# Kernel tuning notes

Hardware: AMD Instinct MI355X
Metric: run time of the kernel (lower is better)

Reference implementation:

```python
import jax, jax.numpy as jnp
import numpy as np


def _gcn_conv(x, W, b, src, dst, num_nodes):
    # PyG GCNConv: linear transform, add self-loops, symmetric normalization,
    # scatter-sum aggregation, then bias.
    h = x @ W  # [N, out]
    loop = jnp.arange(num_nodes, dtype=src.dtype)
    s = jnp.concatenate([src, loop])
    d = jnp.concatenate([dst, loop])
    deg = jax.ops.segment_sum(jnp.ones_like(s, dtype=h.dtype), d, num_segments=num_nodes)
    dinv = jnp.where(deg > 0, jax.lax.rsqrt(deg), 0.0)
    norm = dinv[s] * dinv[d]  # [E+N]
    msgs = h[s] * norm[:, None]  # gather + scale
    out = jax.ops.segment_sum(msgs, d, num_segments=num_nodes)
    return out + b


def setup_inputs() -> dict:
    key = jax.random.key(0)
    k1, k2, k3, k4 = jax.random.split(key, 4)
    N, F_in, H, C, E = 100000, 512, 16, 40, 3200000
    node_feature = jax.random.normal(k1, (N, F_in), dtype=jnp.float32)
    W1 = jax.random.normal(k2, (F_in, H), dtype=jnp.float32) * (1.0 / np.sqrt(F_in))
    b1 = jnp.zeros((H,), dtype=jnp.float32)
    W2 = jax.random.normal(k3, (H, C), dtype=jnp.float32) * (1.0 / np.sqrt(H))
    b2 = jnp.zeros((C,), dtype=jnp.float32)
    edge_index = jax.random.randint(k4, (2, E), 0, N, dtype=jnp.int64)
    return {"node_feature": node_feature, "W1": W1, "b1": b1,
            "W2": W2, "b2": b2, "edge_index": edge_index}


def reference(node_feature, W1, b1, W2, b2, edge_index):
    # Inference path: F.dropout(training=False) is identity.
    N = node_feature.shape[0]
    src, dst = edge_index[0], edge_index[1]
    x = jax.nn.elu(_gcn_conv(node_feature, W1, b1, src, dst, N))
    x = _gcn_conv(x, W2, b2, src, dst, N)
    return jax.nn.log_softmax(x, axis=1)
```

## Files before the change

### kernel.cpp

```cpp
#include <hip/hip_runtime.h>
#include <hip/hip_bf16.h>
#include <math.h>

typedef __attribute__((ext_vector_type(8))) short bf16x8;
typedef __attribute__((ext_vector_type(4))) float f32x4;

#define CAP 8192

__device__ __forceinline__ unsigned pk_bf16(float lo, float hi) {
    unsigned a = __float_as_uint(lo), b = __float_as_uint(hi);
    unsigned alo = (a + 0x7fffu + ((a >> 16) & 1u)) >> 16;
    unsigned bhi = (b + 0x7fffu + ((b >> 16) & 1u)) >> 16;
    return alo | (bhi << 16);
}
__device__ __forceinline__ float bf_lo(unsigned u) { return __uint_as_float(u << 16); }
__device__ __forceinline__ float bf_hi(unsigned u) { return __uint_as_float(u & 0xffff0000u); }


__global__ __launch_bounds__(256) void k_place1(
    const int* __restrict__ src, const int* __restrict__ dst,
    int* __restrict__ gcur, unsigned* __restrict__ ebuf,
    int E, int B, int CHUNK)
{
    __shared__ int hist[1024];
    __shared__ int curb[1024];
    int tid = threadIdx.x, b = blockIdx.x;
    for (int j = tid; j < B; j += 256) hist[j] = 0;
    __syncthreads();
    int e0 = b * CHUNK, e1 = min(e0 + CHUNK, E);
    for (int i = e0 + tid * 4; i < e1; i += 1024) {
        if (i + 3 < e1) {
            int4 d4 = *(const int4*)(dst + i);
            atomicAdd(&hist[d4.x >> 7], 1);
            atomicAdd(&hist[d4.y >> 7], 1);
            atomicAdd(&hist[d4.z >> 7], 1);
            atomicAdd(&hist[d4.w >> 7], 1);
        } else {
            for (int k = i; k < e1; ++k) atomicAdd(&hist[dst[k] >> 7], 1);
        }
    }
    __syncthreads();
    for (int j = tid; j < B; j += 256) {
        int h = hist[j];
        curb[j] = h ? atomicAdd(&gcur[j], h) : 0;
    }
    __syncthreads();
    for (int i = e0 + tid * 4; i < e1; i += 1024) {
        if (i + 3 < e1) {
            int4 d4 = *(const int4*)(dst + i);
            int4 s4 = *(const int4*)(src + i);
            int p0 = atomicAdd(&curb[d4.x >> 7], 1);
            int p1 = atomicAdd(&curb[d4.y >> 7], 1);
            int p2 = atomicAdd(&curb[d4.z >> 7], 1);
            int p3 = atomicAdd(&curb[d4.w >> 7], 1);
            ebuf[(size_t)(d4.x >> 7) * CAP + p0] = ((unsigned)(d4.x & 127) << 17) | (unsigned)s4.x;
            ebuf[(size_t)(d4.y >> 7) * CAP + p1] = ((unsigned)(d4.y & 127) << 17) | (unsigned)s4.y;
            ebuf[(size_t)(d4.z >> 7) * CAP + p2] = ((unsigned)(d4.z & 127) << 17) | (unsigned)s4.z;
            ebuf[(size_t)(d4.w >> 7) * CAP + p3] = ((unsigned)(d4.w & 127) << 17) | (unsigned)s4.w;
        } else {
            for (int k = i; k < e1; ++k) {
                int d = dst[k], s = src[k];
                int pos = atomicAdd(&curb[d >> 7], 1);
                ebuf[(size_t)(d >> 7) * CAP + pos] = ((unsigned)(d & 127) << 17) | (unsigned)s;
            }
        }
    }
}

__global__ __launch_bounds__(256) void k_csr(
    const int* __restrict__ gcur, const unsigned* __restrict__ ebuf,
    int* __restrict__ csr, int2* __restrict__ odeg,
    float* __restrict__ dinv, int N)
{
    __shared__ int sm[128];
    __shared__ int loc[128];
    int j = blockIdx.x, tid = threadIdx.x;
    int e0 = j * CAP;
    int e1 = e0 + gcur[j];
    if (tid < 128) sm[tid] = 0;
    __syncthreads();
    for (int i = e0 + tid; i < e1; i += 256) atomicAdd(&sm[ebuf[i] >> 17], 1);
    __syncthreads();
    int v = (tid < 128) ? sm[tid] : 0;
    for (int off = 1; off < 128; off <<= 1) {
        int t = (tid < 128 && tid >= off) ? sm[tid - off] : 0;
        __syncthreads();
        if (tid < 128) sm[tid] += t;
        __syncthreads();
    }
    if (tid < 128) {
        int ex = sm[tid] - v;
        loc[tid] = e0 + ex;
        int n = j * 128 + tid;
        if (n < N) {
            odeg[n] = make_int2(e0 + ex, v);
            dinv[n] = rsqrtf((float)v + 1.0f);
        }
    }
    __syncthreads();
    for (int i = e0 + tid; i < e1; i += 256) {
        unsigned eb = ebuf[i];
        int pos = atomicAdd(&loc[eb >> 17], 1);
        csr[pos] = (int)(eb & 0x1FFFFu);
    }
}

__global__ __launch_bounds__(256) void k_gemm1(
    const float* __restrict__ x, const float* __restrict__ W1,
    const float* __restrict__ dinv, unsigned* __restrict__ h1s, int N)
{
    const int lane = threadIdx.x & 63;
    const int wid  = threadIdx.x >> 6;
    const int gwave  = blockIdx.x * 4 + wid;
    const int nwaves = gridDim.x * 4;
    const int col = lane & 15;
    const int kg  = lane >> 4;

    unsigned bfr[16][4];
    #pragma unroll
    for (int kk = 0; kk < 16; ++kk) {
        int kbase = kk * 32 + kg * 8;
        #pragma unroll
        for (int i = 0; i < 4; ++i) {
            float lo = W1[(size_t)(kbase + 2 * i) * 16 + col];
            float hi = W1[(size_t)(kbase + 2 * i + 1) * 16 + col];
            bfr[kk][i] = pk_bf16(lo, hi);
        }
    }

    const int TT = N >> 4;
    for (int t = gwave; t < TT; t += nwaves) {
        const float* xr = x + (size_t)(t * 16 + col) * 512 + kg * 8;
        f32x4 acc = {0.f, 0.f, 0.f, 0.f};
        #pragma unroll
        for (int kk = 0; kk < 16; ++kk) {
            float4 xa = *(const float4*)(xr + kk * 32);
            float4 xb = *(const float4*)(xr + kk * 32 + 4);
            unsigned afr[4];
            afr[0] = pk_bf16(xa.x, xa.y);
            afr[1] = pk_bf16(xa.z, xa.w);
            afr[2] = pk_bf16(xb.x, xb.y);
            afr[3] = pk_bf16(xb.z, xb.w);
            acc = __builtin_amdgcn_mfma_f32_16x16x32_bf16(
                *(bf16x8*)afr, *(bf16x8*)&bfr[kk][0], acc, 0, 0, 0);
        }
        float4 dv4 = *(const float4*)(dinv + t * 16 + kg * 4);
        const float* dvp = (const float*)&dv4;
        #pragma unroll
        for (int m = 0; m < 4; ++m) {
            int r = t * 16 + kg * 4 + m;
            float v = acc[m] * dvp[m];
            float oth = __shfl_xor(v, 1);
            if (!(lane & 1))
                h1s[(size_t)r * 8 + (col >> 1)] = pk_bf16(v, oth);
        }
    }
}

__global__ __launch_bounds__(256) void k_l1(
    const int2* __restrict__ odeg, const int* __restrict__ csr,
    const unsigned* __restrict__ h1s, const float* __restrict__ dinv,
    const float* __restrict__ b1, unsigned* __restrict__ x1s, int N)
{
    const int lane = threadIdx.x & 63;
    const int wid  = threadIdx.x >> 6;
    const int gwave  = blockIdx.x * 4 + wid;
    const int nwaves = gridDim.x * 4;
    const int eg = lane >> 3, w = lane & 7;
    const float b1v = b1[lane & 15];

    for (int n = gwave; n < N; n += nwaves) {
        int2 od = odeg[n];
        int o0 = od.x, cnt = od.y;
        float accx = 0.f, accy = 0.f;
        for (int cb = 0; cb < cnt; cb += 64) {
            int cs = cnt - cb; if (cs > 64) cs = 64;
            int sreg = (lane < cs) ? csr[o0 + cb + lane] : 0;
            int iters = (cs + 7) >> 3;
            for (int i = 0; i < iters; ++i) {
                int e = i * 8 + eg;
                int s = __shfl(sreg, e);
                if (e < cs) {
                    unsigned u = h1s[(size_t)s * 8 + w];
                    accx += bf_lo(u);
                    accy += bf_hi(u);
                }
            }
        }
        accx += __shfl_xor(accx, 8);  accy += __shfl_xor(accy, 8);
        accx += __shfl_xor(accx, 16); accy += __shfl_xor(accy, 16);
        accx += __shfl_xor(accx, 32); accy += __shfl_xor(accy, 32);

        float dv = dinv[n];
        float fx = __shfl(accx, lane >> 1), fy = __shfl(accy, lane >> 1);
        float xv = 0.f;
        if (lane < 16) {
            float aggv = (lane & 1) ? fy : fx;
            unsigned su = h1s[(size_t)n * 8 + (lane >> 1)];
            float self = (lane & 1) ? bf_hi(su) : bf_lo(su);
            xv = (aggv + self) * dv + b1v;
            xv = xv > 0.f ? xv : expm1f(xv);
            xv *= dv;
        }
        float oth = __shfl_xor(xv, 1);
        if (lane < 16 && !(lane & 1))
            x1s[(size_t)n * 8 + (lane >> 1)] = pk_bf16(xv, oth);
    }
}

__global__ __launch_bounds__(256) void k_l2(
    const int2* __restrict__ odeg, const int* __restrict__ csr,
    const unsigned* __restrict__ x1s, const float* __restrict__ dinv,
    const float* __restrict__ W2, const float* __restrict__ b2,
    float* __restrict__ out, int N)
{
    const int lane = threadIdx.x & 63;
    const int wid  = threadIdx.x >> 6;
    const int gwave  = blockIdx.x * 4 + wid;
    const int nwaves = gridDim.x * 4;
    const int eg = lane >> 3, w = lane & 7;
    const int c = lane < 40 ? lane : 39;

    float w2[16];
    #pragma unroll
    for (int t = 0; t < 16; ++t) w2[t] = W2[t * 40 + c];
    const float b2v = b2[c];

    for (int n = gwave; n < N; n += nwaves) {
        int2 od = odeg[n];
        int o0 = od.x, cnt = od.y;
        float accx = 0.f, accy = 0.f;
        for (int cb = 0; cb < cnt; cb += 64) {
            int cs = cnt - cb; if (cs > 64) cs = 64;
            int sreg = (lane < cs) ? csr[o0 + cb + lane] : 0;
            int iters = (cs + 7) >> 3;
            for (int i = 0; i < iters; ++i) {
                int e = i * 8 + eg;
                int s = __shfl(sreg, e);
                if (e < cs) {
                    unsigned u = x1s[(size_t)s * 8 + w];
                    accx += bf_lo(u);
                    accy += bf_hi(u);
                }
            }
        }
        accx += __shfl_xor(accx, 8);  accy += __shfl_xor(accy, 8);
        accx += __shfl_xor(accx, 16); accy += __shfl_xor(accy, 16);
        accx += __shfl_xor(accx, 32); accy += __shfl_xor(accy, 32);

        float dv = dinv[n];
        float fx = __shfl(accx, lane >> 1), fy = __shfl(accy, lane >> 1);
        float xv = 0.f;
        if (lane < 16) {
            float aggv = (lane & 1) ? fy : fx;
            unsigned su = x1s[(size_t)n * 8 + (lane >> 1)];
            float self = (lane & 1) ? bf_hi(su) : bf_lo(su);
            xv = (aggv + self) * dv;
        }
        float v = b2v;
        #pragma unroll
        for (int t = 0; t < 16; ++t)
            v = fmaf(__shfl(xv, t), w2[t], v);

        float vm = (lane < 40) ? v : -INFINITY;
        #pragma unroll
        for (int off = 32; off; off >>= 1) vm = fmaxf(vm, __shfl_xor(vm, off));
        float ex = (lane < 40) ? expf(v - vm) : 0.f;
        float sum = ex;
        #pragma unroll
        for (int off = 32; off; off >>= 1) sum += __shfl_xor(sum, off);
        if (lane < 40) out[(size_t)n * 40 + lane] = v - vm - logf(sum);
    }
}

extern "C" void kernel_launch(void* const* d_in, const int* in_sizes, int n_in,
                              void* d_out, int out_size, void* d_ws, size_t ws_size,
                              hipStream_t stream) {
    const float* x  = (const float*)d_in[0];
    const float* W1 = (const float*)d_in[1];
    const float* b1 = (const float*)d_in[2];
    const float* W2 = (const float*)d_in[3];
    const float* b2 = (const float*)d_in[4];
    const int*   ei = (const int*)d_in[5];

    const int N = in_sizes[0] / 512;
    const int E = in_sizes[5] / 2;
    const int* src = ei;
    const int* dst = ei + E;

    const int B     = (N + 127) >> 7;
    const int CHUNK = 16384;
    const int NBLK  = (E + CHUNK - 1) / CHUNK;

    int*      gcur = (int*)d_ws;
    unsigned* ebuf = (unsigned*)(gcur + 1024);
    int*      csr  = (int*)(ebuf + (size_t)B * CAP);
    int2*     odeg = (int2*)(csr + (size_t)B * CAP);
    float*    dinv = (float*)(odeg + N);
    unsigned* h1s  = (unsigned*)(dinv + N);
    unsigned* x1s  = h1s + (size_t)8 * N;
    float*    out  = (float*)d_out;

    const int GB = ((N >> 4) + 3) / 4;

    hipMemsetAsync(gcur, 0, (size_t)B * sizeof(int), stream);

    k_place1<<<NBLK, 256, 0, stream>>>(src, dst, gcur, ebuf, E, B, CHUNK);
    k_csr   <<<B, 256, 0, stream>>>(gcur, ebuf, csr, odeg, dinv, N);
    k_gemm1 <<<GB, 256, 0, stream>>>(x, W1, dinv, h1s, N);
    k_l1    <<<2048, 256, 0, stream>>>(odeg, csr, h1s, dinv, b1, x1s, N);
    k_l2    <<<2048, 256, 0, stream>>>(odeg, csr, x1s, dinv, W2, b2, out, N);
}
```

Baseline: 230.3 us.

## Merge partition stages and both GCN layers into cooperative kernels with grid sync

Replaces the memset, edge placement and CSR build launches with a single cooperative kernel that uses grid.sync between phases. The two aggregation layers are likewise fused into one cooperative persistent kernel, with a grid barrier between layer 1 and layer 2. The aim is to remove kernel launch gaps and the memset. In exchange, grids are sized by occupancy, so the edge chunks become larger, fewer blocks partition the edges, and grid barriers add their own cost. The old multi-kernel path is kept as a fallback if the cooperative launch fails.

Result: slower. 760.1 us (+230.0%).

```diff
diff --git a/kernel.cpp b/kernel.cpp
--- a/kernel.cpp
+++ b/kernel.cpp
@@ -1,6 +1,9 @@
 #include <hip/hip_runtime.h>
+#include <hip/hip_cooperative_groups.h>
 #include <hip/hip_bf16.h>
 #include <math.h>
+
+namespace cg = cooperative_groups;
 
 typedef __attribute__((ext_vector_type(8))) short bf16x8;
 typedef __attribute__((ext_vector_type(4))) float f32x4;
@@ -16,6 +19,99 @@
 __device__ __forceinline__ float bf_lo(unsigned u) { return __uint_as_float(u << 16); }
 __device__ __forceinline__ float bf_hi(unsigned u) { return __uint_as_float(u & 0xffff0000u); }
 
+
+__global__ void k_partition(
+    const int* __restrict__ src, const int* __restrict__ dst,
+    int* __restrict__ gcur, unsigned* __restrict__ ebuf,
+    int* __restrict__ csr, int2* __restrict__ odeg, float* __restrict__ dinv,
+    int E, int B, int N, int CHUNK)
+{
+    cg::grid_group grid = cg::this_grid();
+    __shared__ int hist[1024];
+    __shared__ int curb[1024];
+    const int tid = threadIdx.x;
+
+    for (int z = blockIdx.x * 256 + tid; z < B; z += gridDim.x * 256) gcur[z] = 0;
+    grid.sync();
+
+    const int NCH = (E + CHUNK - 1) / CHUNK;
+    for (int cb = blockIdx.x; cb < NCH; cb += gridDim.x) {
+        for (int j = tid; j < B; j += 256) hist[j] = 0;
+        __syncthreads();
+        int e0 = cb * CHUNK, e1 = min(e0 + CHUNK, E);
+        for (int i = e0 + tid * 4; i < e1; i += 1024) {
+            if (i + 3 < e1) {
+                int4 d4 = *(const int4*)(dst + i);
+                atomicAdd(&hist[d4.x >> 7], 1);
+                atomicAdd(&hist[d4.y >> 7], 1);
+                atomicAdd(&hist[d4.z >> 7], 1);
+                atomicAdd(&hist[d4.w >> 7], 1);
+            } else {
+                for (int k = i; k < e1; ++k) atomicAdd(&hist[dst[k] >> 7], 1);
+            }
+        }
+        __syncthreads();
+        for (int j = tid; j < B; j += 256) {
+            int h = hist[j];
+            curb[j] = h ? atomicAdd(&gcur[j], h) : 0;
+        }
+        __syncthreads();
+        for (int i = e0 + tid * 4; i < e1; i += 1024) {
+            if (i + 3 < e1) {
+                int4 d4 = *(const int4*)(dst + i);
+                int4 s4 = *(const int4*)(src + i);
+                int p0 = atomicAdd(&curb[d4.x >> 7], 1);
+                int p1 = atomicAdd(&curb[d4.y >> 7], 1);
+                int p2 = atomicAdd(&curb[d4.z >> 7], 1);
+                int p3 = atomicAdd(&curb[d4.w >> 7], 1);
+                ebuf[(size_t)(d4.x >> 7) * CAP + p0] = ((unsigned)(d4.x & 127) << 17) | (unsigned)s4.x;
+                ebuf[(size_t)(d4.y >> 7) * CAP + p1] = ((unsigned)(d4.y & 127) << 17) | (unsigned)s4.y;
+                ebuf[(size_t)(d4.z >> 7) * CAP + p2] = ((unsigned)(d4.z & 127) << 17) | (unsigned)s4.z;
+                ebuf[(size_t)(d4.w >> 7) * CAP + p3] = ((unsigned)(d4.w & 127) << 17) | (unsigned)s4.w;
+            } else {
+                for (int k = i; k < e1; ++k) {
+                    int d = dst[k], s = src[k];
+                    int pos = atomicAdd(&curb[d >> 7], 1);
+                    ebuf[(size_t)(d >> 7) * CAP + pos] = ((unsigned)(d & 127) << 17) | (unsigned)s;
+                }
+            }
+        }
+        __syncthreads();
+    }
+    grid.sync();
+
+    for (int jb = blockIdx.x; jb < B; jb += gridDim.x) {
+        int f0 = jb * CAP;
+        int f1 = f0 + gcur[jb];
+        if (tid < 128) hist[tid] = 0;
+        __syncthreads();
+        for (int i = f0 + tid; i < f1; i += 256) atomicAdd(&hist[ebuf[i] >> 17], 1);
+        __syncthreads();
+        int v = (tid < 128) ? hist[tid] : 0;
+        for (int off = 1; off < 128; off <<= 1) {
+            int t = (tid < 128 && tid >= off) ? hist[tid - off] : 0;
+            __syncthreads();
+            if (tid < 128) hist[tid] += t;
+            __syncthreads();
+        }
+        if (tid < 128) {
+            int ex = hist[tid] - v;
+            curb[tid] = f0 + ex;
+            int n = jb * 128 + tid;
+            if (n < N) {
+                odeg[n] = make_int2(f0 + ex, v);
+                dinv[n] = rsqrtf((float)v + 1.0f);
+            }
+        }
+        __syncthreads();
+        for (int i = f0 + tid; i < f1; i += 256) {
+            unsigned eb = ebuf[i];
+            int pos = atomicAdd(&curb[eb >> 17], 1);
+            csr[pos] = (int)(eb & 0x1FFFFu);
+        }
+        __syncthreads();
+    }
+}
 
 __global__ __launch_bounds__(256) void k_place1(
     const int* __restrict__ src, const int* __restrict__ dst,
@@ -157,18 +253,13 @@
     }
 }
 
-__global__ __launch_bounds__(256) void k_l1(
+__device__ __forceinline__ void l1_body(
     const int2* __restrict__ odeg, const int* __restrict__ csr,
     const unsigned* __restrict__ h1s, const float* __restrict__ dinv,
-    const float* __restrict__ b1, unsigned* __restrict__ x1s, int N)
-{
-    const int lane = threadIdx.x & 63;
-    const int wid  = threadIdx.x >> 6;
-    const int gwave  = blockIdx.x * 4 + wid;
-    const int nwaves = gridDim.x * 4;
-    const int eg = lane >> 3, w = lane & 7;
+    const float* __restrict__ b1, unsigned* __restrict__ x1s,
+    int N, int gwave, int nwaves, int lane, int eg, int w)
+{
     const float b1v = b1[lane & 15];
-
     for (int n = gwave; n < N; n += nwaves) {
         int2 od = odeg[n];
         int o0 = od.x, cnt = od.y;
@@ -208,19 +299,13 @@
     }
 }
 
-__global__ __launch_bounds__(256) void k_l2(
+__device__ __forceinline__ void l2_body(
     const int2* __restrict__ odeg, const int* __restrict__ csr,
     const unsigned* __restrict__ x1s, const float* __restrict__ dinv,
     const float* __restrict__ W2, const float* __restrict__ b2,
-    float* __restrict__ out, int N)
-{
-    const int lane = threadIdx.x & 63;
-    const int wid  = threadIdx.x >> 6;
-    const int gwave  = blockIdx.x * 4 + wid;
-    const int nwaves = gridDim.x * 4;
-    const int eg = lane >> 3, w = lane & 7;
+    float* __restrict__ out, int N, int gwave, int nwaves, int lane, int eg, int w)
+{
     const int c = lane < 40 ? lane : 39;
-
     float w2[16];
     #pragma unroll
     for (int t = 0; t < 16; ++t) w2[t] = W2[t * 40 + c];
@@ -273,6 +358,48 @@
     }
 }
 
+__global__ void k_layers(
+    const int2* __restrict__ odeg, const int* __restrict__ csr,
+    const unsigned* __restrict__ h1s, const float* __restrict__ dinv,
+    const float* __restrict__ b1, const float* __restrict__ W2,
+    const float* __restrict__ b2, unsigned* __restrict__ x1s,
+    float* __restrict__ out, int N)
+{
+    cg::grid_group grid = cg::this_grid();
+    const int lane = threadIdx.x & 63;
+    const int wid  = threadIdx.x >> 6;
+    const int gwave  = blockIdx.x * 4 + wid;
+    const int nwaves = gridDim.x * 4;
+    const int eg = lane >> 3, w = lane & 7;
+
+    l1_body(odeg, csr, h1s, dinv, b1, x1s, N, gwave, nwaves, lane, eg, w);
+    grid.sync();
+    l2_body(odeg, csr, x1s, dinv, W2, b2, out, N, gwave, nwaves, lane, eg, w);
+}
+
+__global__ __launch_bounds__(256) void k_l1(
+    const int2* __restrict__ odeg, const int* __restrict__ csr,
+    const unsigned* __restrict__ h1s, const float* __restrict__ dinv,
+    const float* __restrict__ b1, unsigned* __restrict__ x1s, int N)
+{
+    const int lane = threadIdx.x & 63;
+    const int wid  = threadIdx.x >> 6;
+    l1_body(odeg, csr, h1s, dinv, b1, x1s, N,
+            blockIdx.x * 4 + wid, gridDim.x * 4, lane, lane >> 3, lane & 7);
+}
+
+__global__ __launch_bounds__(256) void k_l2(
+    const int2* __restrict__ odeg, const int* __restrict__ csr,
+    const unsigned* __restrict__ x1s, const float* __restrict__ dinv,
+    const float* __restrict__ W2, const float* __restrict__ b2,
+    float* __restrict__ out, int N)
+{
+    const int lane = threadIdx.x & 63;
+    const int wid  = threadIdx.x >> 6;
+    l2_body(odeg, csr, x1s, dinv, W2, b2, out, N,
+            blockIdx.x * 4 + wid, gridDim.x * 4, lane, lane >> 3, lane & 7);
+}
+
 extern "C" void kernel_launch(void* const* d_in, const int* in_sizes, int n_in,
                               void* d_out, int out_size, void* d_ws, size_t ws_size,
                               hipStream_t stream) {
@@ -283,14 +410,12 @@
     const float* b2 = (const float*)d_in[4];
     const int*   ei = (const int*)d_in[5];
 
-    const int N = in_sizes[0] / 512;
-    const int E = in_sizes[5] / 2;
+    int N = in_sizes[0] / 512;
+    int E = in_sizes[5] / 2;
     const int* src = ei;
     const int* dst = ei + E;
 
-    const int B     = (N + 127) >> 7;
-    const int CHUNK = 16384;
-    const int NBLK  = (E + CHUNK - 1) / CHUNK;
+    int B = (N + 127) >> 7;
 
     int*      gcur = (int*)d_ws;
     unsigned* ebuf = (unsigned*)(gcur + 1024);
@@ -303,11 +428,52 @@
 
     const int GB = ((N >> 4) + 3) / 4;
 
-    hipMemsetAsync(gcur, 0, (size_t)B * sizeof(int), stream);
-
-    k_place1<<<NBLK, 256, 0, stream>>>(src, dst, gcur, ebuf, E, B, CHUNK);
-    k_csr   <<<B, 256, 0, stream>>>(gcur, ebuf, csr, odeg, dinv, N);
-    k_gemm1 <<<GB, 256, 0, stream>>>(x, W1, dinv, h1s, N);
-    k_l1    <<<2048, 256, 0, stream>>>(odeg, csr, h1s, dinv, b1, x1s, N);
-    k_l2    <<<2048, 256, 0, stream>>>(odeg, csr, x1s, dinv, W2, b2, out, N);
-}
+    int dev = 0;  hipGetDevice(&dev);
+    int numCU = 0;
+    hipDeviceGetAttribute(&numCU, hipDeviceAttributeMultiprocessorCount, dev);
+    if (numCU <= 0) numCU = 256;
+    int occA = 0, occB = 0;
+    bool coop = true;
+    if (hipOccupancyMaxActiveBlocksPerMultiprocessor(&occA, k_partition, 256, 0) != hipSuccess || occA <= 0) coop = false;
+    if (hipOccupancyMaxActiveBlocksPerMultiprocessor(&occB, k_layers, 256, 0) != hipSuccess || occB <= 0) coop = false;
+
+    bool partition_done = false, layers_done = false;
+    int GA = 0, CH = 0, GL = 0;
+    if (coop) {
+        GA = occA * numCU; if (GA > 2048) GA = 2048;
+        CH = (((E + GA - 1) / GA) + 3) & ~3;
+        void* argsA[] = {(void*)&src, (void*)&dst, (void*)&gcur, (void*)&ebuf,
+                         (void*)&csr, (void*)&odeg, (void*)&dinv,
+                         (void*)&E, (void*)&B, (void*)&N, (void*)&CH};
+        if (hipLaunchCooperativeKernel((void*)k_partition, dim3(GA), dim3(256),
+                                       argsA, 0, stream) == hipSuccess)
+            partition_done = true;
+        else
+            (void)hipGetLastError();
+    }
+    if (!partition_done) {
+        const int CHUNK = 16384;
+        const int NBLK  = (E + CHUNK - 1) / CHUNK;
+        hipMemsetAsync(gcur, 0, (size_t)B * sizeof(int), stream);
+        k_place1<<<NBLK, 256, 0, stream>>>(src, dst, gcur, ebuf, E, B, CHUNK);
+        k_csr   <<<B, 256, 0, stream>>>(gcur, ebuf, csr, odeg, dinv, N);
+    }
+
+    k_gemm1<<<GB, 256, 0, stream>>>(x, W1, dinv, h1s, N);
+
+    if (coop) {
+        GL = occB * numCU; if (GL > 2048) GL = 2048;
+        void* argsB[] = {(void*)&odeg, (void*)&csr, (void*)&h1s, (void*)&dinv,
+                         (void*)&b1, (void*)&W2, (void*)&b2, (void*)&x1s,
+                         (void*)&out, (void*)&N};
+        if (hipLaunchCooperativeKernel((void*)k_layers, dim3(GL), dim3(256),
+                                       argsB, 0, stream) == hipSuccess)
+            layers_done = true;
+        else
+            (void)hipGetLastError();
+    }
+    if (!layers_done) {
+        k_l1<<<2048, 256, 0, stream>>>(odeg, csr, h1s, dinv, b1, x1s, N);
+        k_l2<<<2048, 256, 0, stream>>>(odeg, csr, x1s, dinv, W2, b2, out, N);
+    }
+}
```
